# Performance work log

Hardware: AMD Instinct MI355X
Metric: run time of the kernel (lower is better)

Reference implementation:

```python
import jax, jax.numpy as jnp
import numpy as np

N = 100000   # nodes
E = 1600000  # edges
B = 4096     # graphs
F_IN = 92
H = 51       # hidden_channels
ED = 10      # edge_dim
T = 7        # num_timesteps

def _p(key, shape, scale=0.1):
    return scale * jax.random.normal(key, shape, dtype=jnp.float32)

def setup_inputs():
    key = jax.random.key(0)
    ks = jax.random.split(key, 20)
    return {
        "x": jax.random.normal(ks[0], (N, F_IN), dtype=jnp.float32),
        "edge_index": jax.random.randint(ks[1], (2, E), 0, N),
        "edge_attr": jax.random.normal(ks[2], (E, ED), dtype=jnp.float32),
        "batch": jnp.sort(jax.random.randint(ks[3], (N,), 0, B)),
        "W1": _p(ks[4], (F_IN, H)), "b1": jnp.zeros((H,), jnp.float32),
        "We1": _p(ks[5], (H + ED, H)),
        "att_l": _p(ks[6], (H,)), "att_r": _p(ks[7], (H,)),
        "We2": _p(ks[8], (H, H)), "gate_bias": jnp.zeros((H,), jnp.float32),
        "Wih1": _p(ks[9], (H, 3 * H)), "bih1": jnp.zeros((3 * H,), jnp.float32),
        "Whh1": _p(ks[10], (H, 3 * H)), "bhh1": jnp.zeros((3 * H,), jnp.float32),
        "Wm": _p(ks[11], (H, H)),
        "att_src": _p(ks[12], (H,)), "att_dst": _p(ks[13], (H,)),
        "mol_bias": jnp.zeros((H,), jnp.float32),
        "Wih2": _p(ks[14], (H, 3 * H)), "bih2": jnp.zeros((3 * H,), jnp.float32),
        "Whh2": _p(ks[15], (H, 3 * H)), "bhh2": jnp.zeros((3 * H,), jnp.float32),
        "W2": _p(ks[16], (H, 1)), "b2": jnp.zeros((1,), jnp.float32),
    }

def _lrelu(v):
    return jax.nn.leaky_relu(v, 0.01)

def _seg_softmax(a, idx, num):
    # scatter-softmax over segments (PyG softmax with 1e-16 denom eps)
    m = jax.ops.segment_max(a, idx, num_segments=num)
    e = jnp.exp(a - m[idx])
    s = jax.ops.segment_sum(e, idx, num_segments=num)
    return e / (s[idx] + 1e-16)

def _gru(xin, h, Wih, bih, Whh, bhh):
    # torch.nn.GRUCell, gate order r, z, n
    gi = xin @ Wih + bih
    gh = h @ Whh + bhh
    ir, iz, inn = jnp.split(gi, 3, axis=-1)
    hr, hz, hn = jnp.split(gh, 3, axis=-1)
    r = jax.nn.sigmoid(ir + hr)
    z = jax.nn.sigmoid(iz + hz)
    n = jnp.tanh(inn + r * hn)
    return (1.0 - z) * n + z * h

def reference(x, edge_index, edge_attr, batch, W1, b1, We1, att_l, att_r, We2,
              gate_bias, Wih1, bih1, Whh1, bhh1, Wm, att_src, att_dst, mol_bias,
              Wih2, bih2, Whh2, bhh2, W2, b2):
    src, dst = edge_index[0], edge_index[1]
    # AttentiveFP.lin1 + leaky_relu
    x = _lrelu(x @ W1 + b1)                                        # (N, H)
    # GATEConv: edge-conditioned attention, aggregate to dst
    xe = _lrelu(jnp.concatenate([x[src], edge_attr], axis=-1) @ We1)  # (E, H)
    a = _lrelu(xe @ att_l + x[dst] @ att_r)                        # (E,)
    alpha = _seg_softmax(a, dst, N)
    h = jax.ops.segment_sum((xe @ We2) * alpha[:, None], dst, num_segments=N) + gate_bias
    h = jax.nn.elu(h)                                              # dropout off (eval)
    x = jax.nn.relu(_gru(h, x, Wih1, bih1, Whh1, bhh1))            # (N, H)
    # molecule readout: GATConv over bipartite (nodes -> graphs) edges (arange(N), batch)
    out = jax.nn.relu(jax.ops.segment_sum(x, batch, num_segments=B))  # (B, H)
    xl = x @ Wm                                                    # (N, H), constant over t
    al = xl @ att_src                                              # (N,)
    for _ in range(T):
        ar = (out @ Wm) @ att_dst                                  # (B,)
        a = _lrelu(al + ar[batch])
        alpha = _seg_softmax(a, batch, B)
        hm = jax.ops.segment_sum(xl * alpha[:, None], batch, num_segments=B) + mol_bias
        hm = jax.nn.elu(hm)
        out = jax.nn.relu(_gru(hm, out, Wih2, bih2, Whh2, bhh2))
    return out @ W2 + b2                                           # (B, 1)
```

## Files before the change

kernel.cpp:

```cpp
#include <hip/hip_runtime.h>
#include <stdint.h>

#define NN 100000
#define NE 1600000
#define NB 4096
#define FIN 92
#define H 51
#define H3 153
#define TSTEPS 7
#define SCAN_B 391
#define GG_BLOCKS 768
#define GG_CHUNKS (NN / 32)

__device__ __align__(16) float g_x1[(size_t)NN * 52 + 64];
__device__ __align__(16) unsigned short g_pb[(size_t)NN * 52 + 64];
__device__ float g_xr[NN];
__device__ float g_agg[(size_t)NN * H + 64];
__device__ float g_x2[(size_t)NN * H + 64];
__device__ float g_xl[(size_t)NN * H + 64];
__device__ float g_al[NN];
__device__ int   g_gs[NB + 2];
__device__ float g_wg1[H * H * 8];
__device__ float g_bg1[64 * 8];
__device__ float g_wg2[H * H * 8];
__device__ float g_bg2[64 * 8];
__device__ float g_wv[64];
__device__ int   g_cnt[NN];
__device__ int   g_rp[NN + 1];
__device__ int   g_cur[NN];
__device__ int   g_src[NE + 4];
__device__ __align__(16) uint32_t g_eac[(size_t)NE * 6 + 16];
__device__ int   g_bsum[512];
__device__ int   g_boff[512];

__device__ __forceinline__ float lrelu(float v) { return v > 0.f ? v : 0.01f * v; }
__device__ __forceinline__ float elu1(float v) { return v > 0.f ? v : expm1f(v); }
__device__ __forceinline__ float sigm(float v) { return 1.f / (1.f + __expf(-v)); }

__device__ __forceinline__ float bflo(uint32_t w) { union { uint32_t u; float f; } c; c.u = w << 16; return c.f; }
__device__ __forceinline__ float bfhi(uint32_t w) { union { uint32_t u; float f; } c; c.u = w & 0xffff0000u; return c.f; }
__device__ __forceinline__ uint32_t f2bf(float f) {
    uint32_t u = __float_as_uint(f);
    return (u + 0x7FFFu + ((u >> 16) & 1u)) >> 16;
}

__device__ __forceinline__ float wave_sum(float v) {
    v += __shfl_xor(v, 32, 64);
    v += __shfl_xor(v, 16, 64);
    v += __shfl_xor(v, 8, 64);
    v += __shfl_xor(v, 4, 64);
    v += __shfl_xor(v, 2, 64);
    v += __shfl_xor(v, 1, 64);
    return v;
}
__device__ __forceinline__ void wave_sum4(float& a, float& b, float& c, float& d) {
    a += __shfl_xor(a, 32, 64); b += __shfl_xor(b, 32, 64); c += __shfl_xor(c, 32, 64); d += __shfl_xor(d, 32, 64);
    a += __shfl_xor(a, 16, 64); b += __shfl_xor(b, 16, 64); c += __shfl_xor(c, 16, 64); d += __shfl_xor(d, 16, 64);
    a += __shfl_xor(a, 8, 64);  b += __shfl_xor(b, 8, 64);  c += __shfl_xor(c, 8, 64);  d += __shfl_xor(d, 8, 64);
    a += __shfl_xor(a, 4, 64);  b += __shfl_xor(b, 4, 64);  c += __shfl_xor(c, 4, 64);  d += __shfl_xor(d, 4, 64);
    a += __shfl_xor(a, 2, 64);  b += __shfl_xor(b, 2, 64);  c += __shfl_xor(c, 2, 64);  d += __shfl_xor(d, 2, 64);
    a += __shfl_xor(a, 1, 64);  b += __shfl_xor(b, 1, 64);  c += __shfl_xor(c, 1, 64);  d += __shfl_xor(d, 1, 64);
}

__global__ __launch_bounds__(256) void k_init(const int* __restrict__ batch) {
    int n = blockIdx.x * 256 + threadIdx.x;
    if (n >= NN) return;
    g_cnt[n] = 0;
    int bn = batch[n];
    int bp = (n == 0) ? -1 : batch[n - 1];
    for (int b = bp + 1; b <= bn; ++b) g_gs[b] = n;
    if (n == NN - 1) for (int b = bn + 1; b <= NB; ++b) g_gs[b] = NN;
}

__global__ void k_prep(const float* __restrict__ Wih1, const float* __restrict__ bih1,
                       const float* __restrict__ Whh1, const float* __restrict__ bhh1,
                       const float* __restrict__ Wih2, const float* __restrict__ bih2,
                       const float* __restrict__ Whh2, const float* __restrict__ bhh2,
                       const float* __restrict__ Wm, const float* __restrict__ ad) {
    int id = blockIdx.x * 256 + threadIdx.x;
    int which = 0;
    const float *Wih, *bih, *Whh, *bhh;
    if (id < H * H) {
        which = 0; Wih = Wih1; bih = bih1; Whh = Whh1; bhh = bhh1;
    } else if (id < 2 * H * H) {
        which = 1; id -= H * H; Wih = Wih2; bih = bih2; Whh = Whh2; bhh = bhh2;
    } else {
        int k = id - 2 * H * H;
        if (k < 64) {
            float a = 0.f;
            if (k < H) for (int j = 0; j < H; ++j) a = fmaf(Wm[k * H + j], ad[j], a);
            g_wv[k] = a;
        }
        return;
    }
    float* Wg = which ? g_wg2 : g_wg1;
    float* bg = which ? g_bg2 : g_bg1;
    int k = id / H, j = id - k * H;
    float* o = Wg + (size_t)id * 8;
    o[0] = Wih[k * H3 + j];
    o[1] = Wih[k * H3 + H + j];
    o[2] = Wih[k * H3 + 2 * H + j];
    o[3] = Whh[k * H3 + j];
    o[4] = Whh[k * H3 + H + j];
    o[5] = Whh[k * H3 + 2 * H + j];
    o[6] = 0.f; o[7] = 0.f;
    if (id < H) {
        float* ob = bg + (size_t)id * 8;
        ob[0] = bih[id]; ob[1] = bih[H + id]; ob[2] = bih[2 * H + id];
        ob[3] = bhh[id]; ob[4] = bhh[H + id]; ob[5] = bhh[2 * H + id];
        ob[6] = 0.f; ob[7] = 0.f;
    }
}

__global__ __launch_bounds__(256) void k_count(const int* __restrict__ ei) {
    int e = blockIdx.x * 256 + threadIdx.x;
    if (e >= NE) return;
    atomicAdd(&g_cnt[ei[NE + e]], 1);
}

__global__ __launch_bounds__(256) void k_scan1() {
    __shared__ int sm[256];
    int tid = threadIdx.x;
    int i = blockIdx.x * 256 + tid;
    sm[tid] = (i < NN) ? g_cnt[i] : 0;
    __syncthreads();
#pragma unroll
    for (int off = 1; off < 256; off <<= 1) {
        int t = (tid >= off) ? sm[tid - off] : 0;
        __syncthreads();
        sm[tid] += t;
        __syncthreads();
    }
    if (i < NN) g_rp[i + 1] = sm[tid];
    if (tid == 255) g_bsum[blockIdx.x] = sm[255];
}

__global__ void k_scan2() {
    __shared__ int sm[512];
    int tid = threadIdx.x;
    sm[tid] = (tid < SCAN_B) ? g_bsum[tid] : 0;
    __syncthreads();
#pragma unroll
    for (int off = 1; off < 512; off <<= 1) {
        int t = (tid >= off) ? sm[tid - off] : 0;
        __syncthreads();
        sm[tid] += t;
        __syncthreads();
    }
    if (tid < SCAN_B) g_boff[tid] = (tid == 0) ? 0 : sm[tid - 1];
}

__global__ __launch_bounds__(256) void k_scan3() {
    int i = blockIdx.x * 256 + threadIdx.x;
    if (i >= NN) return;
    int v = g_rp[i + 1] + g_boff[blockIdx.x];
    g_rp[i + 1] = v;
    if (i == 0) { g_rp[0] = 0; g_cur[0] = 0; }
    if (i + 1 < NN) g_cur[i + 1] = v;
}

__global__ __launch_bounds__(256) void k_fill(const int* __restrict__ ei, const float* __restrict__ ea) {
    int e = blockIdx.x * 256 + threadIdx.x;
    if (e >= NE) return;
    int d = ei[NE + e];
    int pos = atomicAdd(&g_cur[d], 1);
    g_src[pos] = ei[e];
    const float2* s2 = (const float2*)(ea + (size_t)e * 10);
    float2 v0 = s2[0], v1 = s2[1], v2 = s2[2], v3 = s2[3], v4 = s2[4];
    uint32_t d0 = f2bf(v0.x) | (f2bf(v0.y) << 16);
    uint32_t d1 = f2bf(v1.x) | (f2bf(v1.y) << 16);
    uint32_t d2 = f2bf(v2.x) | (f2bf(v2.y) << 16);
    uint32_t d3 = f2bf(v3.x) | (f2bf(v3.y) << 16);
    uint32_t d4 = f2bf(v4.x) | (f2bf(v4.y) << 16);
    uint2* dp = (uint2*)(g_eac + (size_t)pos * 6);
    dp[0] = make_uint2(d0, d1);
    dp[1] = make_uint2(d2, d3);
    dp[2] = make_uint2(d4, 0u);
}

__global__ __launch_bounds__(256, 3) void k_lin1(const float* __restrict__ x, const float* __restrict__ W1,
                                                 const float* __restrict__ b1, const float* __restrict__ attr_,
                                                 const float* __restrict__ We1) {
    int n = blockIdx.x * 256 + threadIdx.x;
    if (n >= NN) return;
    const float4* xq4 = (const float4*)(x + (size_t)n * FIN);
    float acc[H];
#pragma unroll
    for (int h = 0; h < H; ++h) acc[h] = 0.f;
#pragma unroll 1
    for (int q = 0; q < FIN / 4; ++q) {
        float4 v = xq4[q];
        const float* wr = W1 + (4 * q) * H;
#pragma unroll
        for (int h = 0; h < H; ++h)
            acc[h] = fmaf(v.x, wr[h], fmaf(v.y, wr[H + h], fmaf(v.z, wr[2 * H + h], fmaf(v.w, wr[3 * H + h], acc[h]))));
    }
    float xrv = 0.f;
    float* xo = g_x1 + (size_t)n * 52;
#pragma unroll
    for (int h = 0; h < H; ++h) {
        float v = lrelu(acc[h] + b1[h]);
        acc[h] = v;
        xo[h] = v;
        xrv = fmaf(v, attr_[h], xrv);
    }
    xo[H] = 0.f;
    g_xr[n] = xrv;
    unsigned short* po = g_pb + (size_t)n * 52;
#pragma unroll 1
    for (int h = 0; h < H; ++h) {
        float ph = 0.f;
#pragma unroll
        for (int k = 0; k < H; ++k) ph = fmaf(acc[k], We1[k * H + h], ph);
        po[h] = (unsigned short)f2bf(ph);
    }
    po[H] = 0;
}

__global__ __launch_bounds__(256, 4) void k_gate(const float* __restrict__ We1, const float* __restrict__ attl) {
    int lane = threadIdx.x & 63;
    int lj = lane < H ? lane : H - 1;
    int n = __builtin_amdgcn_readfirstlane(blockIdx.x * 4 + (threadIdx.x >> 6));
    float we0 = We1[(51 + 0) * H + lj], we1 = We1[(51 + 1) * H + lj];
    float we2 = We1[(51 + 2) * H + lj], we3 = We1[(51 + 3) * H + lj];
    float we4 = We1[(51 + 4) * H + lj], we5 = We1[(51 + 5) * H + lj];
    float we6 = We1[(51 + 6) * H + lj], we7 = We1[(51 + 7) * H + lj];
    float we8 = We1[(51 + 8) * H + lj], we9 = We1[(51 + 9) * H + lj];
    float attlv = attl[lj];
    float xrd = g_xr[n];
    int rs = g_rp[n], re = g_rp[n + 1];
    float accH = 0.f, den = 0.f;
    int nb = (re - rs) >> 2;
    int idx = rs;
    float pv0 = 0.f, pv1 = 0.f, pv2 = 0.f, pv3 = 0.f;
    if (nb > 0) {
        int s0 = __builtin_amdgcn_readfirstlane(g_src[idx]);
        int s1 = __builtin_amdgcn_readfirstlane(g_src[idx + 1]);
        int s2 = __builtin_amdgcn_readfirstlane(g_src[idx + 2]);
        int s3 = __builtin_amdgcn_readfirstlane(g_src[idx + 3]);
        pv0 = bflo(g_pb[(size_t)s0 * 52 + lane]);
        pv1 = bflo(g_pb[(size_t)s1 * 52 + lane]);
        pv2 = bflo(g_pb[(size_t)s2 * 52 + lane]);
        pv3 = bflo(g_pb[(size_t)s3 * 52 + lane]);
    }
#pragma unroll 1
    for (int blk = 0; blk < nb; ++blk) {
        int ci = idx;
        float cp0 = pv0, cp1 = pv1, cp2 = pv2, cp3 = pv3;
        idx += 4;
        if (blk + 1 < nb) {
            int s0 = __builtin_amdgcn_readfirstlane(g_src[idx]);
            int s1 = __builtin_amdgcn_readfirstlane(g_src[idx + 1]);
            int s2 = __builtin_amdgcn_readfirstlane(g_src[idx + 2]);
            int s3 = __builtin_amdgcn_readfirstlane(g_src[idx + 3]);
            pv0 = bflo(g_pb[(size_t)s0 * 52 + lane]);
            pv1 = bflo(g_pb[(size_t)s1 * 52 + lane]);
            pv2 = bflo(g_pb[(size_t)s2 * 52 + lane]);
            pv3 = bflo(g_pb[(size_t)s3 * 52 + lane]);
        }
        const uint2* ep0 = (const uint2*)(g_eac + (size_t)ci * 6);
        const uint2* ep1 = (const uint2*)(g_eac + (size_t)(ci + 1) * 6);
        const uint2* ep2 = (const uint2*)(g_eac + (size_t)(ci + 2) * 6);
        const uint2* ep3 = (const uint2*)(g_eac + (size_t)(ci + 3) * 6);
        uint2 A0 = ep0[0], B0 = ep0[1], C0 = ep0[2];
        uint2 A1 = ep1[0], B1 = ep1[1], C1 = ep1[2];
        uint2 A2 = ep2[0], B2 = ep2[1], C2 = ep2[2];
        uint2 A3 = ep3[0], B3 = ep3[1], C3 = ep3[2];
        float xe0 = cp0, xe1 = cp1, xe2 = cp2, xe3 = cp3;
        xe0 = fmaf(bflo(A0.x), we0, xe0); xe0 = fmaf(bfhi(A0.x), we1, xe0);
        xe0 = fmaf(bflo(A0.y), we2, xe0); xe0 = fmaf(bfhi(A0.y), we3, xe0);
        xe0 = fmaf(bflo(B0.x), we4, xe0); xe0 = fmaf(bfhi(B0.x), we5, xe0);
        xe0 = fmaf(bflo(B0.y), we6, xe0); xe0 = fmaf(bfhi(B0.y), we7, xe0);
        xe0 = fmaf(bflo(C0.x), we8, xe0); xe0 = fmaf(bfhi(C0.x), we9, xe0);
        xe1 = fmaf(bflo(A1.x), we0, xe1); xe1 = fmaf(bfhi(A1.x), we1, xe1);
        xe1 = fmaf(bflo(A1.y), we2, xe1); xe1 = fmaf(bfhi(A1.y), we3, xe1);
        xe1 = fmaf(bflo(B1.x), we4, xe1); xe1 = fmaf(bfhi(B1.x), we5, xe1);
        xe1 = fmaf(bflo(B1.y), we6, xe1); xe1 = fmaf(bfhi(B1.y), we7, xe1);
        xe1 = fmaf(bflo(C1.x), we8, xe1); xe1 = fmaf(bfhi(C1.x), we9, xe1);
        xe2 = fmaf(bflo(A2.x), we0, xe2); xe2 = fmaf(bfhi(A2.x), we1, xe2);
        xe2 = fmaf(bflo(A2.y), we2, xe2); xe2 = fmaf(bfhi(A2.y), we3, xe2);
        xe2 = fmaf(bflo(B2.x), we4, xe2); xe2 = fmaf(bfhi(B2.x), we5, xe2);
        xe2 = fmaf(bflo(B2.y), we6, xe2); xe2 = fmaf(bfhi(B2.y), we7, xe2);
        xe2 = fmaf(bflo(C2.x), we8, xe2); xe2 = fmaf(bfhi(C2.x), we9, xe2);
        xe3 = fmaf(bflo(A3.x), we0, xe3); xe3 = fmaf(bfhi(A3.x), we1, xe3);
        xe3 = fmaf(bflo(A3.y), we2, xe3); xe3 = fmaf(bfhi(A3.y), we3, xe3);
        xe3 = fmaf(bflo(B3.x), we4, xe3); xe3 = fmaf(bfhi(B3.x), we5, xe3);
        xe3 = fmaf(bflo(B3.y), we6, xe3); xe3 = fmaf(bfhi(B3.y), we7, xe3);
        xe3 = fmaf(bflo(C3.x), we8, xe3); xe3 = fmaf(bfhi(C3.x), we9, xe3);
        float l0 = lrelu(xe0), l1 = lrelu(xe1), l2 = lrelu(xe2), l3 = lrelu(xe3);
        float p0 = (lane < H) ? l0 * attlv : 0.f;
        float p1 = (lane < H) ? l1 * attlv : 0.f;
        float p2 = (lane < H) ? l2 * attlv : 0.f;
        float p3 = (lane < H) ? l3 * attlv : 0.f;
        wave_sum4(p0, p1, p2, p3);
        float e0 = __expf(lrelu(p0 + xrd));
        float e1 = __expf(lrelu(p1 + xrd));
        float e2 = __expf(lrelu(p2 + xrd));
        float e3 = __expf(lrelu(p3 + xrd));
        accH = fmaf(e0, l0, accH); den += e0;
        accH = fmaf(e1, l1, accH); den += e1;
        accH = fmaf(e2, l2, accH); den += e2;
        accH = fmaf(e3, l3, accH); den += e3;
    }
    for (; idx < re; ++idx) {
        int s0 = __builtin_amdgcn_readfirstlane(g_src[idx]);
        float pvs = bflo(g_pb[(size_t)s0 * 52 + lane]);
        const uint2* ep0 = (const uint2*)(g_eac + (size_t)idx * 6);
        uint2 A0 = ep0[0], B0 = ep0[1], C0 = ep0[2];
        float xe0 = pvs;
        xe0 = fmaf(bflo(A0.x), we0, xe0); xe0 = fmaf(bfhi(A0.x), we1, xe0);
        xe0 = fmaf(bflo(A0.y), we2, xe0); xe0 = fmaf(bfhi(A0.y), we3, xe0);
        xe0 = fmaf(bflo(B0.x), we4, xe0); xe0 = fmaf(bfhi(B0.x), we5, xe0);
        xe0 = fmaf(bflo(B0.y), we6, xe0); xe0 = fmaf(bfhi(B0.y), we7, xe0);
        xe0 = fmaf(bflo(C0.x), we8, xe0); xe0 = fmaf(bfhi(C0.x), we9, xe0);
        float l0 = lrelu(xe0);
        float a0 = wave_sum((lane < H) ? l0 * attlv : 0.f);
        float e0 = __expf(lrelu(a0 + xrd));
        accH = fmaf(e0, l0, accH); den += e0;
    }
    if (lane < H) g_agg[(size_t)n * H + lane] = accH / (den + 1e-16f);
}

__global__ __launch_bounds__(256) void k_gategru(const float* __restrict__ We2, const float* __restrict__ gb,
                                                 const float* __restrict__ Wm, const float* __restrict__ asrc) {
    __shared__ uint32_t wA[H * H];
    __shared__ uint32_t wB[H * H];
    __shared__ uint32_t wC[H * H];
    __shared__ float lA[4][52][8];
    __shared__ float lX[4][52][8];
    __shared__ float lH[4][52][8];
    int tid = threadIdx.x;
    for (int i = tid; i < H * H; i += 256) {
        const float* s = g_wg1 + (size_t)i * 8;
        wA[i] = f2bf(s[0]) | (f2bf(s[1]) << 16);
        wB[i] = f2bf(s[2]) | (f2bf(s[3]) << 16);
        wC[i] = f2bf(s[4]) | (f2bf(s[5]) << 16);
    }
    __syncthreads();
    int w = tid >> 6;
    int lane = tid & 63;
    int lj = lane < H ? lane : H - 1;
    const float4* bp = (const float4*)(g_bg1 + lane * 8);
    float4 b0 = bp[0];
    float4 b1v = bp[1];
    float gbl = gb[lj];
    float asl = asrc[lj];
#pragma unroll 1
    for (int chunk = blockIdx.x; chunk < GG_CHUNKS; chunk += GG_BLOCKS) {
        int base = __builtin_amdgcn_readfirstlane(chunk * 32 + w * 8);
        float xj[8], ag[8];
#pragma unroll
        for (int m = 0; m < 8; ++m) {
            xj[m] = g_x1[(size_t)(base + m) * 52 + lane];
            ag[m] = g_agg[(size_t)(base + m) * H + lane];
        }
        if (lane < H) {
#pragma unroll
            for (int m = 0; m < 8; ++m) { lA[w][lane][m] = ag[m]; lX[w][lane][m] = xj[m]; }
        }
        float ac[8];
#pragma unroll
        for (int m = 0; m < 8; ++m) ac[m] = 0.f;
#pragma unroll 1
        for (int k = 0; k < H; ++k) {
            float wv = We2[k * H + lj];
            float4 a0 = *(const float4*)&lA[w][k][0];
            float4 a1 = *(const float4*)&lA[w][k][4];
            ac[0] = fmaf(a0.x, wv, ac[0]); ac[1] = fmaf(a0.y, wv, ac[1]);
            ac[2] = fmaf(a0.z, wv, ac[2]); ac[3] = fmaf(a0.w, wv, ac[3]);
            ac[4] = fmaf(a1.x, wv, ac[4]); ac[5] = fmaf(a1.y, wv, ac[5]);
            ac[6] = fmaf(a1.z, wv, ac[6]); ac[7] = fmaf(a1.w, wv, ac[7]);
        }
        float hb[8];
#pragma unroll
        for (int m = 0; m < 8; ++m) hb[m] = elu1(ac[m] + gbl);
        if (lane < H) {
#pragma unroll
            for (int m = 0; m < 8; ++m) lH[w][lane][m] = hb[m];
        }
        float gir[8], giz[8], gin[8], ghr[8], ghz[8], ghn[8];
#pragma unroll
        for (int m = 0; m < 8; ++m) { gir[m] = 0; giz[m] = 0; gin[m] = 0; ghr[m] = 0; ghz[m] = 0; ghn[m] = 0; }
#pragma unroll 1
        for (int k = 0; k < H; ++k) {
            uint32_t wa = wA[k * H + lj];
            uint32_t wb = wB[k * H + lj];
            uint32_t wc = wC[k * H + lj];
            float w0x = bflo(wa), w0y = bfhi(wa), w0z = bflo(wb);
            float w0w = bfhi(wb), w1x = bflo(wc), w1y = bfhi(wc);
            float4 h0 = *(const float4*)&lH[w][k][0];
            float4 h1 = *(const float4*)&lH[w][k][4];
            float4 x0 = *(const float4*)&lX[w][k][0];
            float4 x1v = *(const float4*)&lX[w][k][4];
            float hk[8] = { h0.x, h0.y, h0.z, h0.w, h1.x, h1.y, h1.z, h1.w };
            float xk[8] = { x0.x, x0.y, x0.z, x0.w, x1v.x, x1v.y, x1v.z, x1v.w };
#pragma unroll
            for (int m = 0; m < 8; ++m) {
                gir[m] = fmaf(hk[m], w0x, gir[m]); giz[m] = fmaf(hk[m], w0y, giz[m]); gin[m] = fmaf(hk[m], w0z, gin[m]);
                ghr[m] = fmaf(xk[m], w0w, ghr[m]); ghz[m] = fmaf(xk[m], w1x, ghz[m]); ghn[m] = fmaf(xk[m], w1y, ghn[m]);
            }
        }
        float o2[8];
#pragma unroll
        for (int m = 0; m < 8; ++m) {
            float r = sigm(gir[m] + b0.x + ghr[m] + b0.w);
            float z = sigm(giz[m] + b0.y + ghz[m] + b1v.x);
            float nn2 = tanhf(gin[m] + b0.z + r * (ghn[m] + b1v.y));
            o2[m] = fmaxf((1.f - z) * nn2 + z * xj[m], 0.f);
            if (lane < H) g_x2[(size_t)(base + m) * H + lane] = o2[m];
        }
        if (lane < H) {
#pragma unroll
            for (int m = 0; m < 8; ++m) lH[w][lane][m] = o2[m];
        }
        float xl[8];
#pragma unroll
        for (int m = 0; m < 8; ++m) xl[m] = 0.f;
#pragma unroll 1
        for (int k = 0; k < H; ++k) {
            float wv = Wm[k * H + lj];
            float4 o0 = *(const float4*)&lH[w][k][0];
            float4 o1 = *(const float4*)&lH[w][k][4];
            xl[0] = fmaf(o0.x, wv, xl[0]); xl[1] = fmaf(o0.y, wv, xl[1]);
            xl[2] = fmaf(o0.z, wv, xl[2]); xl[3] = fmaf(o0.w, wv, xl[3]);
            xl[4] = fmaf(o1.x, wv, xl[4]); xl[5] = fmaf(o1.y, wv, xl[5]);
            xl[6] = fmaf(o1.z, wv, xl[6]); xl[7] = fmaf(o1.w, wv, xl[7]);
        }
        float v0, v1, v2, v3, v4, v5, v6, v7;
        v0 = (lane < H) ? xl[0] * asl : 0.f;
        v1 = (lane < H) ? xl[1] * asl : 0.f;
        v2 = (lane < H) ? xl[2] * asl : 0.f;
        v3 = (lane < H) ? xl[3] * asl : 0.f;
        v4 = (lane < H) ? xl[4] * asl : 0.f;
        v5 = (lane < H) ? xl[5] * asl : 0.f;
        v6 = (lane < H) ? xl[6] * asl : 0.f;
        v7 = (lane < H) ? xl[7] * asl : 0.f;
        wave_sum4(v0, v1, v2, v3);
        wave_sum4(v4, v5, v6, v7);
#pragma unroll
        for (int m = 0; m < 8; ++m)
            if (lane < H) g_xl[(size_t)(base + m) * H + lane] = xl[m];
        if (lane == 0) {
            g_al[base + 0] = v0; g_al[base + 1] = v1; g_al[base + 2] = v2; g_al[base + 3] = v3;
            g_al[base + 4] = v4; g_al[base + 5] = v5; g_al[base + 6] = v6; g_al[base + 7] = v7;
        }
    }
}

__global__ __launch_bounds__(256) void k_mol_all(const float* __restrict__ mb, const float* __restrict__ W2,
                                                 const float* __restrict__ b2, float* __restrict__ dout) {
    __shared__ uint32_t ldsWa[H * H];
    __shared__ uint32_t ldsWb[H * H];
    __shared__ uint32_t ldsWc[H * H];
    __shared__ float lbc[4][52][2];
    int tid = threadIdx.x;
    for (int i = tid; i < H * H; i += 256) {
        const float* s = g_wg2 + (size_t)i * 8;
        ldsWa[i] = f2bf(s[0]) | (f2bf(s[1]) << 16);
        ldsWb[i] = f2bf(s[2]) | (f2bf(s[3]) << 16);
        ldsWc[i] = f2bf(s[4]) | (f2bf(s[5]) << 16);
    }
    __syncthreads();
    int w = tid >> 6;
    int lane = tid & 63;
    int lj = lane < H ? lane : H - 1;
    int b = __builtin_amdgcn_readfirstlane(blockIdx.x * 4 + w);
    int gs = g_gs[b], ge = g_gs[b + 1];
    float oa = 0.f, ob = 0.f;
    int i = gs;
    for (; i + 2 <= ge; i += 2) {
        oa += g_x2[(size_t)i * H + lane];
        ob += g_x2[(size_t)(i + 1) * H + lane];
    }
    if (i < ge) oa += g_x2[(size_t)i * H + lane];
    float oj = fmaxf(oa + ob, 0.f);
    float wvl = g_wv[lane];
    float mbl = mb[lj];
    const float4* bp = (const float4*)(g_bg2 + lane * 8);
    float4 b0 = bp[0];
    float4 b1v = bp[1];
#pragma unroll 1
    for (int t = 0; t < TSTEPS; ++t) {
        float arb = wave_sum((lane < H) ? oj * wvl : 0.f);
        float sa = 0.f, sb = 0.f, aa = 0.f, ab = 0.f;
        i = gs;
        for (; i + 2 <= ge; i += 2) {
            float ev0 = __expf(lrelu(g_al[i] + arb));
            float ev1 = __expf(lrelu(g_al[i + 1] + arb));
            sa += ev0; sb += ev1;
            aa = fmaf(ev0, g_xl[(size_t)i * H + lane], aa);
            ab = fmaf(ev1, g_xl[(size_t)(i + 1) * H + lane], ab);
        }
        if (i < ge) {
            float ev0 = __expf(lrelu(g_al[i] + arb));
            sa += ev0;
            aa = fmaf(ev0, g_xl[(size_t)i * H + lane], aa);
        }
        float inv = 1.f / (sa + sb + 1e-16f);
        float hm = elu1((aa + ab) * inv + mbl);
        if (lane < H) { lbc[w][lane][0] = hm; lbc[w][lane][1] = oj; }
        float gir = 0, giz = 0, gin = 0, ghr = 0, ghz = 0, ghn = 0;
#pragma unroll 2
        for (int k = 0; k < H; ++k) {
            uint32_t wa = ldsWa[k * H + lj];
            uint32_t wb = ldsWb[k * H + lj];
            uint32_t wc = ldsWc[k * H + lj];
            float2 ho = *(const float2*)&lbc[w][k][0];
            float hmk = ho.x, ok = ho.y;
            gir = fmaf(hmk, bflo(wa), gir); giz = fmaf(hmk, bfhi(wa), giz); gin = fmaf(hmk, bflo(wb), gin);
            ghr = fmaf(ok, bfhi(wb), ghr);  ghz = fmaf(ok, bflo(wc), ghz);  ghn = fmaf(ok, bfhi(wc), ghn);
        }
        float r = sigm(gir + b0.x + ghr + b0.w);
        float z = sigm(giz + b0.y + ghz + b1v.x);
        float nn2 = tanhf(gin + b0.z + r * (ghn + b1v.y));
        oj = fmaxf((1.f - z) * nn2 + z * oj, 0.f);
    }
    float fv = wave_sum((lane < H) ? oj * W2[lj] : 0.f);
    if (lane == 0) dout[b] = fv + b2[0];
}

extern "C" void kernel_launch(void* const* d_in, const int* in_sizes, int n_in,
                              void* d_out, int out_size, void* d_ws, size_t ws_size,
                              hipStream_t stream) {
    const float* x     = (const float*)d_in[0];
    const int*   ei    = (const int*)d_in[1];
    const float* ea    = (const float*)d_in[2];
    const int*   batch = (const int*)d_in[3];
    const float* W1    = (const float*)d_in[4];
    const float* b1    = (const float*)d_in[5];
    const float* We1   = (const float*)d_in[6];
    const float* attl  = (const float*)d_in[7];
    const float* attr_ = (const float*)d_in[8];
    const float* We2   = (const float*)d_in[9];
    const float* gb    = (const float*)d_in[10];
    const float* Wm    = (const float*)d_in[15];
    const float* asrc  = (const float*)d_in[16];
    const float* adst  = (const float*)d_in[17];
    const float* mb    = (const float*)d_in[18];
    const float* W2    = (const float*)d_in[23];
    const float* b2    = (const float*)d_in[24];
    float* dout = (float*)d_out;

    k_init<<<SCAN_B, 256, 0, stream>>>(batch);
    k_count<<<NE / 256, 256, 0, stream>>>(ei);
    k_scan1<<<SCAN_B, 256, 0, stream>>>();
    k_scan2<<<1, 512, 0, stream>>>();
    k_scan3<<<SCAN_B, 256, 0, stream>>>();
    k_fill<<<NE / 256, 256, 0, stream>>>(ei, ea);

    k_prep<<<(2 * H * H + 64 + 255) / 256, 256, 0, stream>>>(
        (const float*)d_in[11], (const float*)d_in[12], (const float*)d_in[13], (const float*)d_in[14],
        (const float*)d_in[19], (const float*)d_in[20], (const float*)d_in[21], (const float*)d_in[22],
        Wm, adst);

    k_lin1<<<(NN + 255) / 256, 256, 0, stream>>>(x, W1, b1, attr_, We1);
    k_gate<<<NN / 4, 256, 0, stream>>>(We1, attl);
    k_gategru<<<GG_BLOCKS, 256, 0, stream>>>(We2, gb, Wm, asrc);
    k_mol_all<<<NB / 4, 256, 0, stream>>>(mb, W2, b2, dout);
}
```

Measured before the change: 570.3 us.

## Drop LDS weight staging in gate-GRU kernel and launch one block per chunk

The GRU gate weights are now packed to bf16 once in k_prep and read straight from global memory/L1 in the k_gategru inner loop, instead of being staged into about 31KB of LDS per block. LDS buffers shrink by reusing a single temp array, which should raise occupancy. The persistent grid-stride loop is replaced by one block per 32-node chunk (3125 blocks). This trades LDS reads for global/cache reads of the weights in the hot loop, and adds s_barrier calls around the reuse of the temp buffer.

```diff
diff --git a/kernel.cpp b/kernel.cpp
--- a/kernel.cpp
+++ b/kernel.cpp
@@ -9,7 +9,6 @@
 #define H3 153
 #define TSTEPS 7
 #define SCAN_B 391
-#define GG_BLOCKS 768
 #define GG_CHUNKS (NN / 32)
 
 __device__ __align__(16) float g_x1[(size_t)NN * 52 + 64];
@@ -20,7 +19,9 @@
 __device__ float g_xl[(size_t)NN * H + 64];
 __device__ float g_al[NN];
 __device__ int   g_gs[NB + 2];
-__device__ float g_wg1[H * H * 8];
+__device__ uint32_t g_w1a[H * H];
+__device__ uint32_t g_w1b[H * H];
+__device__ uint32_t g_w1c[H * H];
 __device__ float g_bg1[64 * 8];
 __device__ float g_wg2[H * H * 8];
 __device__ float g_bg2[64 * 8];
@@ -78,37 +79,49 @@
                        const float* __restrict__ Whh2, const float* __restrict__ bhh2,
                        const float* __restrict__ Wm, const float* __restrict__ ad) {
     int id = blockIdx.x * 256 + threadIdx.x;
-    int which = 0;
-    const float *Wih, *bih, *Whh, *bhh;
     if (id < H * H) {
-        which = 0; Wih = Wih1; bih = bih1; Whh = Whh1; bhh = bhh1;
-    } else if (id < 2 * H * H) {
-        which = 1; id -= H * H; Wih = Wih2; bih = bih2; Whh = Whh2; bhh = bhh2;
-    } else {
-        int k = id - 2 * H * H;
-        if (k < 64) {
-            float a = 0.f;
-            if (k < H) for (int j = 0; j < H; ++j) a = fmaf(Wm[k * H + j], ad[j], a);
-            g_wv[k] = a;
+        int k = id / H, j = id - k * H;
+        float w0 = Wih1[k * H3 + j];
+        float w1 = Wih1[k * H3 + H + j];
+        float w2 = Wih1[k * H3 + 2 * H + j];
+        float w3 = Whh1[k * H3 + j];
+        float w4 = Whh1[k * H3 + H + j];
+        float w5 = Whh1[k * H3 + 2 * H + j];
+        g_w1a[id] = f2bf(w0) | (f2bf(w1) << 16);
+        g_w1b[id] = f2bf(w2) | (f2bf(w3) << 16);
+        g_w1c[id] = f2bf(w4) | (f2bf(w5) << 16);
+        if (id < H) {
+            float* ob = g_bg1 + (size_t)id * 8;
+            ob[0] = bih1[id]; ob[1] = bih1[H + id]; ob[2] = bih1[2 * H + id];
+            ob[3] = bhh1[id]; ob[4] = bhh1[H + id]; ob[5] = bhh1[2 * H + id];
+            ob[6] = 0.f; ob[7] = 0.f;
         }
         return;
     }
-    float* Wg = which ? g_wg2 : g_wg1;
-    float* bg = which ? g_bg2 : g_bg1;
-    int k = id / H, j = id - k * H;
-    float* o = Wg + (size_t)id * 8;
-    o[0] = Wih[k * H3 + j];
-    o[1] = Wih[k * H3 + H + j];
-    o[2] = Wih[k * H3 + 2 * H + j];
-    o[3] = Whh[k * H3 + j];
-    o[4] = Whh[k * H3 + H + j];
-    o[5] = Whh[k * H3 + 2 * H + j];
-    o[6] = 0.f; o[7] = 0.f;
-    if (id < H) {
-        float* ob = bg + (size_t)id * 8;
-        ob[0] = bih[id]; ob[1] = bih[H + id]; ob[2] = bih[2 * H + id];
-        ob[3] = bhh[id]; ob[4] = bhh[H + id]; ob[5] = bhh[2 * H + id];
-        ob[6] = 0.f; ob[7] = 0.f;
+    if (id < 2 * H * H) {
+        id -= H * H;
+        int k = id / H, j = id - k * H;
+        float* o = g_wg2 + (size_t)id * 8;
+        o[0] = Wih2[k * H3 + j];
+        o[1] = Wih2[k * H3 + H + j];
+        o[2] = Wih2[k * H3 + 2 * H + j];
+        o[3] = Whh2[k * H3 + j];
+        o[4] = Whh2[k * H3 + H + j];
+        o[5] = Whh2[k * H3 + 2 * H + j];
+        o[6] = 0.f; o[7] = 0.f;
+        if (id < H) {
+            float* ob = g_bg2 + (size_t)id * 8;
+            ob[0] = bih2[id]; ob[1] = bih2[H + id]; ob[2] = bih2[2 * H + id];
+            ob[3] = bhh2[id]; ob[4] = bhh2[H + id]; ob[5] = bhh2[2 * H + id];
+            ob[6] = 0.f; ob[7] = 0.f;
+        }
+        return;
+    }
+    int k = id - 2 * H * H;
+    if (k < 64) {
+        float a = 0.f;
+        if (k < H) for (int j = 0; j < H; ++j) a = fmaf(Wm[k * H + j], ad[j], a);
+        g_wv[k] = a;
     }
 }
 
@@ -323,20 +336,9 @@
 
 __global__ __launch_bounds__(256) void k_gategru(const float* __restrict__ We2, const float* __restrict__ gb,
                                                  const float* __restrict__ Wm, const float* __restrict__ asrc) {
-    __shared__ uint32_t wA[H * H];
-    __shared__ uint32_t wB[H * H];
-    __shared__ uint32_t wC[H * H];
-    __shared__ float lA[4][52][8];
+    __shared__ float lT[4][52][8];
     __shared__ float lX[4][52][8];
-    __shared__ float lH[4][52][8];
     int tid = threadIdx.x;
-    for (int i = tid; i < H * H; i += 256) {
-        const float* s = g_wg1 + (size_t)i * 8;
-        wA[i] = f2bf(s[0]) | (f2bf(s[1]) << 16);
-        wB[i] = f2bf(s[2]) | (f2bf(s[3]) << 16);
-        wC[i] = f2bf(s[4]) | (f2bf(s[5]) << 16);
-    }
-    __syncthreads();
     int w = tid >> 6;
     int lane = tid & 63;
     int lj = lane < H ? lane : H - 1;
@@ -345,105 +347,104 @@
     float4 b1v = bp[1];
     float gbl = gb[lj];
     float asl = asrc[lj];
-#pragma unroll 1
-    for (int chunk = blockIdx.x; chunk < GG_CHUNKS; chunk += GG_BLOCKS) {
-        int base = __builtin_amdgcn_readfirstlane(chunk * 32 + w * 8);
-        float xj[8], ag[8];
+    int base = __builtin_amdgcn_readfirstlane(blockIdx.x * 32 + w * 8);
+    float xj[8], ag[8];
+#pragma unroll
+    for (int m = 0; m < 8; ++m) {
+        xj[m] = g_x1[(size_t)(base + m) * 52 + lane];
+        ag[m] = g_agg[(size_t)(base + m) * H + lane];
+    }
+    if (lane < H) {
+#pragma unroll
+        for (int m = 0; m < 8; ++m) { lT[w][lane][m] = ag[m]; lX[w][lane][m] = xj[m]; }
+    }
+    float ac[8];
+#pragma unroll
+    for (int m = 0; m < 8; ++m) ac[m] = 0.f;
+#pragma unroll 1
+    for (int k = 0; k < H; ++k) {
+        float wv = We2[k * H + lj];
+        float4 a0 = *(const float4*)&lT[w][k][0];
+        float4 a1 = *(const float4*)&lT[w][k][4];
+        ac[0] = fmaf(a0.x, wv, ac[0]); ac[1] = fmaf(a0.y, wv, ac[1]);
+        ac[2] = fmaf(a0.z, wv, ac[2]); ac[3] = fmaf(a0.w, wv, ac[3]);
+        ac[4] = fmaf(a1.x, wv, ac[4]); ac[5] = fmaf(a1.y, wv, ac[5]);
+        ac[6] = fmaf(a1.z, wv, ac[6]); ac[7] = fmaf(a1.w, wv, ac[7]);
+    }
+    float hb[8];
+#pragma unroll
+    for (int m = 0; m < 8; ++m) hb[m] = elu1(ac[m] + gbl);
+    __builtin_amdgcn_s_barrier();
+    if (lane < H) {
+#pragma unroll
+        for (int m = 0; m < 8; ++m) lT[w][lane][m] = hb[m];
+    }
+    float gir[8], giz[8], gin[8], ghr[8], ghz[8], ghn[8];
+#pragma unroll
+    for (int m = 0; m < 8; ++m) { gir[m] = 0; giz[m] = 0; gin[m] = 0; ghr[m] = 0; ghz[m] = 0; ghn[m] = 0; }
+#pragma unroll 1
+    for (int k = 0; k < H; ++k) {
+        uint32_t wa = g_w1a[k * H + lj];
+        uint32_t wb = g_w1b[k * H + lj];
+        uint32_t wc = g_w1c[k * H + lj];
+        float w0x = bflo(wa), w0y = bfhi(wa), w0z = bflo(wb);
+        float w0w = bfhi(wb), w1x = bflo(wc), w1y = bfhi(wc);
+        float4 h0 = *(const float4*)&lT[w][k][0];
+        float4 h1 = *(const float4*)&lT[w][k][4];
+        float4 x0 = *(const float4*)&lX[w][k][0];
+        float4 x1v = *(const float4*)&lX[w][k][4];
+        float hk[8] = { h0.x, h0.y, h0.z, h0.w, h1.x, h1.y, h1.z, h1.w };
+        float xk[8] = { x0.x, x0.y, x0.z, x0.w, x1v.x, x1v.y, x1v.z, x1v.w };
 #pragma unroll
         for (int m = 0; m < 8; ++m) {
-            xj[m] = g_x1[(size_t)(base + m) * 52 + lane];
-            ag[m] = g_agg[(size_t)(base + m) * H + lane];
-        }
-        if (lane < H) {
-#pragma unroll
-            for (int m = 0; m < 8; ++m) { lA[w][lane][m] = ag[m]; lX[w][lane][m] = xj[m]; }
-        }
-        float ac[8];
-#pragma unroll
-        for (int m = 0; m < 8; ++m) ac[m] = 0.f;
-#pragma unroll 1
-        for (int k = 0; k < H; ++k) {
-            float wv = We2[k * H + lj];
-            float4 a0 = *(const float4*)&lA[w][k][0];
-            float4 a1 = *(const float4*)&lA[w][k][4];
-            ac[0] = fmaf(a0.x, wv, ac[0]); ac[1] = fmaf(a0.y, wv, ac[1]);
-            ac[2] = fmaf(a0.z, wv, ac[2]); ac[3] = fmaf(a0.w, wv, ac[3]);
-            ac[4] = fmaf(a1.x, wv, ac[4]); ac[5] = fmaf(a1.y, wv, ac[5]);
-            ac[6] = fmaf(a1.z, wv, ac[6]); ac[7] = fmaf(a1.w, wv, ac[7]);
-        }
-        float hb[8];
-#pragma unroll
-        for (int m = 0; m < 8; ++m) hb[m] = elu1(ac[m] + gbl);
-        if (lane < H) {
-#pragma unroll
-            for (int m = 0; m < 8; ++m) lH[w][lane][m] = hb[m];
-        }
-        float gir[8], giz[8], gin[8], ghr[8], ghz[8], ghn[8];
-#pragma unroll
-        for (int m = 0; m < 8; ++m) { gir[m] = 0; giz[m] = 0; gin[m] = 0; ghr[m] = 0; ghz[m] = 0; ghn[m] = 0; }
-#pragma unroll 1
-        for (int k = 0; k < H; ++k) {
-            uint32_t wa = wA[k * H + lj];
-            uint32_t wb = wB[k * H + lj];
-            uint32_t wc = wC[k * H + lj];
-            float w0x = bflo(wa), w0y = bfhi(wa), w0z = bflo(wb);
-            float w0w = bfhi(wb), w1x = bflo(wc), w1y = bfhi(wc);
-            float4 h0 = *(const float4*)&lH[w][k][0];
-            float4 h1 = *(const float4*)&lH[w][k][4];
-            float4 x0 = *(const float4*)&lX[w][k][0];
-            float4 x1v = *(const float4*)&lX[w][k][4];
-            float hk[8] = { h0.x, h0.y, h0.z, h0.w, h1.x, h1.y, h1.z, h1.w };
-            float xk[8] = { x0.x, x0.y, x0.z, x0.w, x1v.x, x1v.y, x1v.z, x1v.w };
-#pragma unroll
-            for (int m = 0; m < 8; ++m) {
-                gir[m] = fmaf(hk[m], w0x, gir[m]); giz[m] = fmaf(hk[m], w0y, giz[m]); gin[m] = fmaf(hk[m], w0z, gin[m]);
-                ghr[m] = fmaf(xk[m], w0w, ghr[m]); ghz[m] = fmaf(xk[m], w1x, ghz[m]); ghn[m] = fmaf(xk[m], w1y, ghn[m]);
-            }
-        }
-        float o2[8];
-#pragma unroll
-        for (int m = 0; m < 8; ++m) {
-            float r = sigm(gir[m] + b0.x + ghr[m] + b0.w);
-            float z = sigm(giz[m] + b0.y + ghz[m] + b1v.x);
-            float nn2 = tanhf(gin[m] + b0.z + r * (ghn[m] + b1v.y));
-            o2[m] = fmaxf((1.f - z) * nn2 + z * xj[m], 0.f);
-            if (lane < H) g_x2[(size_t)(base + m) * H + lane] = o2[m];
-        }
-        if (lane < H) {
-#pragma unroll
-            for (int m = 0; m < 8; ++m) lH[w][lane][m] = o2[m];
-        }
-        float xl[8];
-#pragma unroll
-        for (int m = 0; m < 8; ++m) xl[m] = 0.f;
-#pragma unroll 1
-        for (int k = 0; k < H; ++k) {
-            float wv = Wm[k * H + lj];
-            float4 o0 = *(const float4*)&lH[w][k][0];
-            float4 o1 = *(const float4*)&lH[w][k][4];
-            xl[0] = fmaf(o0.x, wv, xl[0]); xl[1] = fmaf(o0.y, wv, xl[1]);
-            xl[2] = fmaf(o0.z, wv, xl[2]); xl[3] = fmaf(o0.w, wv, xl[3]);
-            xl[4] = fmaf(o1.x, wv, xl[4]); xl[5] = fmaf(o1.y, wv, xl[5]);
-            xl[6] = fmaf(o1.z, wv, xl[6]); xl[7] = fmaf(o1.w, wv, xl[7]);
-        }
-        float v0, v1, v2, v3, v4, v5, v6, v7;
-        v0 = (lane < H) ? xl[0] * asl : 0.f;
-        v1 = (lane < H) ? xl[1] * asl : 0.f;
-        v2 = (lane < H) ? xl[2] * asl : 0.f;
-        v3 = (lane < H) ? xl[3] * asl : 0.f;
-        v4 = (lane < H) ? xl[4] * asl : 0.f;
-        v5 = (lane < H) ? xl[5] * asl : 0.f;
-        v6 = (lane < H) ? xl[6] * asl : 0.f;
-        v7 = (lane < H) ? xl[7] * asl : 0.f;
-        wave_sum4(v0, v1, v2, v3);
-        wave_sum4(v4, v5, v6, v7);
-#pragma unroll
-        for (int m = 0; m < 8; ++m)
-            if (lane < H) g_xl[(size_t)(base + m) * H + lane] = xl[m];
-        if (lane == 0) {
-            g_al[base + 0] = v0; g_al[base + 1] = v1; g_al[base + 2] = v2; g_al[base + 3] = v3;
-            g_al[base + 4] = v4; g_al[base + 5] = v5; g_al[base + 6] = v6; g_al[base + 7] = v7;
-        }
+            gir[m] = fmaf(hk[m], w0x, gir[m]); giz[m] = fmaf(hk[m], w0y, giz[m]); gin[m] = fmaf(hk[m], w0z, gin[m]);
+            ghr[m] = fmaf(xk[m], w0w, ghr[m]); ghz[m] = fmaf(xk[m], w1x, ghz[m]); ghn[m] = fmaf(xk[m], w1y, ghn[m]);
+        }
+    }
+    float o2[8];
+#pragma unroll
+    for (int m = 0; m < 8; ++m) {
+        float r = sigm(gir[m] + b0.x + ghr[m] + b0.w);
+        float z = sigm(giz[m] + b0.y + ghz[m] + b1v.x);
+        float nn2 = tanhf(gin[m] + b0.z + r * (ghn[m] + b1v.y));
+        o2[m] = fmaxf((1.f - z) * nn2 + z * xj[m], 0.f);
+        if (lane < H) g_x2[(size_t)(base + m) * H + lane] = o2[m];
+    }
+    __builtin_amdgcn_s_barrier();
+    if (lane < H) {
+#pragma unroll
+        for (int m = 0; m < 8; ++m) lT[w][lane][m] = o2[m];
+    }
+    float xl[8];
+#pragma unroll
+    for (int m = 0; m < 8; ++m) xl[m] = 0.f;
+#pragma unroll 1
+    for (int k = 0; k < H; ++k) {
+        float wv = Wm[k * H + lj];
+        float4 o0 = *(const float4*)&lT[w][k][0];
+        float4 o1 = *(const float4*)&lT[w][k][4];
+        xl[0] = fmaf(o0.x, wv, xl[0]); xl[1] = fmaf(o0.y, wv, xl[1]);
+        xl[2] = fmaf(o0.z, wv, xl[2]); xl[3] = fmaf(o0.w, wv, xl[3]);
+        xl[4] = fmaf(o1.x, wv, xl[4]); xl[5] = fmaf(o1.y, wv, xl[5]);
+        xl[6] = fmaf(o1.z, wv, xl[6]); xl[7] = fmaf(o1.w, wv, xl[7]);
+    }
+    float v0, v1, v2, v3, v4, v5, v6, v7;
+    v0 = (lane < H) ? xl[0] * asl : 0.f;
+    v1 = (lane < H) ? xl[1] * asl : 0.f;
+    v2 = (lane < H) ? xl[2] * asl : 0.f;
+    v3 = (lane < H) ? xl[3] * asl : 0.f;
+    v4 = (lane < H) ? xl[4] * asl : 0.f;
+    v5 = (lane < H) ? xl[5] * asl : 0.f;
+    v6 = (lane < H) ? xl[6] * asl : 0.f;
+    v7 = (lane < H) ? xl[7] * asl : 0.f;
+    wave_sum4(v0, v1, v2, v3);
+    wave_sum4(v4, v5, v6, v7);
+#pragma unroll
+    for (int m = 0; m < 8; ++m)
+        if (lane < H) g_xl[(size_t)(base + m) * H + lane] = xl[m];
+    if (lane == 0) {
+        g_al[base + 0] = v0; g_al[base + 1] = v1; g_al[base + 2] = v2; g_al[base + 3] = v3;
+        g_al[base + 4] = v4; g_al[base + 5] = v5; g_al[base + 6] = v6; g_al[base + 7] = v7;
     }
 }
 
@@ -555,6 +556,6 @@
 
     k_lin1<<<(NN + 255) / 256, 256, 0, stream>>>(x, W1, b1, attr_, We1);
     k_gate<<<NN / 4, 256, 0, stream>>>(We1, attl);
-    k_gategru<<<GG_BLOCKS, 256, 0, stream>>>(We2, gb, Wm, asrc);
+    k_gategru<<<GG_CHUNKS, 256, 0, stream>>>(We2, gb, Wm, asrc);
     k_mol_all<<<NB / 4, 256, 0, stream>>>(mb, W2, b2, dout);
 }
```

After: 588.2 us. 3.1% more time.
